# Performance work log

Hardware: AMD Instinct MI355X
Metric: run time of the kernel (lower is better)

## Reference

```python
import jax, jax.numpy as jnp
import numpy as np

N = 100_000      # nodes
E = 1_600_000    # edges (avg degree 16)
IN_DIM = 256
HID = 128
N_OUT = 2


def _linear_params(key, fan_in, fan_out):
    kw, kb = jax.random.split(key)
    bound = 1.0 / np.sqrt(fan_in)
    W = jax.random.uniform(kw, (fan_in, fan_out), jnp.float32, -bound, bound)
    b = jax.random.uniform(kb, (fan_out,), jnp.float32, -bound, bound)
    return W, b


def setup_inputs() -> dict:
    key = jax.random.key(0)
    ks = jax.random.split(key, 6)
    edge_index = jax.random.randint(ks[0], (2, E), 0, N, dtype=jnp.int64)
    x = jax.random.normal(ks[1], (N, IN_DIM), jnp.float32)
    Wi, bi = _linear_params(ks[2], IN_DIM, HID)   # NodeInitializer.lin
    W1, b1 = _linear_params(ks[3], HID, HID)      # GCNConv 1
    W2, b2 = _linear_params(ks[4], HID, HID)      # GCNConv 2
    Wh, bh = _linear_params(ks[5], HID, N_OUT)    # head
    return {"edge_index": edge_index, "x": x, "Wi": Wi, "bi": bi,
            "W1": W1, "b1": b1, "W2": W2, "b2": b2, "Wh": Wh, "bh": bh}


def reference(edge_index, x, Wi, bi, W1, b1, W2, b2, Wh, bh):
    n = x.shape[0]
    # GCNConv preprocessing: add self-loops, symmetric degree normalization.
    loops = jnp.arange(n, dtype=edge_index.dtype)
    src = jnp.concatenate([edge_index[0], loops])  # message source
    dst = jnp.concatenate([edge_index[1], loops])  # aggregation target
    deg = jax.ops.segment_sum(jnp.ones(src.shape[0], jnp.float32), dst, num_segments=n)
    dinv = jnp.where(deg > 0, deg ** -0.5, 0.0)
    norm = dinv[src] * dinv[dst]                   # [E+N]

    # NodeInitializer: relu(linear(x)); dropout = identity (eval mode)
    h = jax.nn.relu(x @ Wi + bi)

    # Two GCNConv layers (no relu between, matching SimpleGCN.forward)
    for W, b in ((W1, b1), (W2, b2)):
        msg = (h @ W)[src] * norm[:, None]         # gather + normalize, [E+N, HID]
        h = jax.ops.segment_sum(msg, dst, num_segments=n) + b  # scatter-add

    return h @ Wh + bh                             # [N, N_OUT]
```

## Files before the change

### kernel.cpp

```cpp
#include <hip/hip_runtime.h>
#include <hip/hip_bf16.h>

#define N_NODES 100000
#define N_EDGES 1600000
#define DIM_IN  256
#define DIM_H   128

#define NBKT 782
#define CPAD 16
#define EPB  8192
#define NBLK ((N_EDGES + EPB - 1) / EPB)

typedef __attribute__((ext_vector_type(8))) short short8;
typedef __attribute__((ext_vector_type(4))) float f32x4;

__device__ __forceinline__ int get_src(const int* e, int is64, int i) {
  return is64 ? e[2 * i] : e[i];
}
__device__ __forceinline__ int get_dst(const int* e, int is64, int i) {
  return is64 ? e[2 * (N_EDGES + i)] : e[N_EDGES + i];
}

__global__ __launch_bounds__(1024)
void k_init(const int* __restrict__ e, int* __restrict__ flag,
            int* __restrict__ bcnt) {
  if (blockIdx.x == 0) {
    __shared__ int s;
    if (threadIdx.x == 0) s = 0;
    __syncthreads();
    atomicOr(&s, e[2 * threadIdx.x + 1]);
    __syncthreads();
    if (threadIdx.x == 0) *flag = (s == 0) ? 1 : 0;
  } else {
    int i = (blockIdx.x - 1) * 1024 + threadIdx.x;
    if (i < NBKT * CPAD) bcnt[i] = 0;
  }
}

__global__ __launch_bounds__(256) void k_zero(int* __restrict__ p, int n) {
  int i = blockIdx.x * 256 + threadIdx.x;
  if (i < n) p[i] = 0;
}

__global__ __launch_bounds__(1024)
void k_binc(const int* __restrict__ eidx, const int* __restrict__ flag,
            int* __restrict__ bcnt) {
  __shared__ int hist[NBKT];
  const int t = threadIdx.x;
  const int is64 = *flag;
  for (int i = t; i < NBKT; i += 1024) hist[i] = 0;
  __syncthreads();
#pragma unroll
  for (int j = 0; j < EPB / 1024; ++j) {
    int e = blockIdx.x * EPB + j * 1024 + t;
    if (e < N_EDGES) {
      unsigned s = (unsigned)get_src(eidx, is64, e);
      unsigned d = (unsigned)get_dst(eidx, is64, e);
      if (s < N_NODES && d < N_NODES) atomicAdd(&hist[d >> 7], 1);
    }
  }
  __syncthreads();
  for (int i = t; i < NBKT; i += 1024) {
    int h = hist[i];
    if (h) atomicAdd(&bcnt[i * CPAD], h);
  }
}

__global__ __launch_bounds__(1024)
void k_bscan(int* __restrict__ bcnt, int* __restrict__ bbase) {
  __shared__ int sm[1024];
  int t = threadIdx.x;
  int v = (t < NBKT) ? bcnt[t * CPAD] : 0;
  sm[t] = v;
  __syncthreads();
  for (int d = 1; d < 1024; d <<= 1) {
    int u = (t >= d) ? sm[t - d] : 0;
    __syncthreads();
    sm[t] += u;
    __syncthreads();
  }
  if (t < NBKT) {
    int excl = sm[t] - v;
    bbase[t] = excl;
    bcnt[t * CPAD] = excl;
    if (t == NBKT - 1) bbase[NBKT] = sm[t];
  }
}

__global__ __launch_bounds__(1024)
void k_bin(const int* __restrict__ eidx, const int* __restrict__ flag,
           int* __restrict__ bcnt, unsigned* __restrict__ ebuf) {
  __shared__ int hist[NBKT];
  __shared__ int cur[NBKT];
  const int t = threadIdx.x;
  const int is64 = *flag;
  for (int i = t; i < NBKT; i += 1024) hist[i] = 0;
  unsigned rec[EPB / 1024];
  int bkt[EPB / 1024];
  __syncthreads();
#pragma unroll
  for (int j = 0; j < EPB / 1024; ++j) {
    int e = blockIdx.x * EPB + j * 1024 + t;
    bkt[j] = -1;
    rec[j] = 0;
    if (e < N_EDGES) {
      unsigned s = (unsigned)get_src(eidx, is64, e);
      unsigned d = (unsigned)get_dst(eidx, is64, e);
      if (s < N_NODES && d < N_NODES) {
        bkt[j] = (int)(d >> 7);
        rec[j] = s | ((d & 127u) << 17);
        atomicAdd(&hist[bkt[j]], 1);
      }
    }
  }
  __syncthreads();
  for (int i = t; i < NBKT; i += 1024) {
    int h = hist[i];
    cur[i] = h ? atomicAdd(&bcnt[i * CPAD], h) : 0;
  }
  __syncthreads();
#pragma unroll
  for (int j = 0; j < EPB / 1024; ++j) {
    if (bkt[j] >= 0) {
      int pos = atomicAdd(&cur[bkt[j]], 1);
      ebuf[pos] = rec[j];
    }
  }
}

__global__ __launch_bounds__(256)
void k_csr(const int* __restrict__ bbase, const unsigned* __restrict__ ebuf,
           int* __restrict__ off, float* __restrict__ dinv,
           int* __restrict__ csr) {
  __shared__ int hist[128];
  __shared__ int scn[128];
  __shared__ int cur[128];
  const int b = blockIdx.x, t = threadIdx.x;
  const int n0 = b << 7;
  const int start = bbase[b], end = bbase[b + 1];
  if (t < 128) hist[t] = 0;
  __syncthreads();
  for (int i = start + t; i < end; i += 256) {
    atomicAdd(&hist[ebuf[i] >> 17], 1);
  }
  __syncthreads();
  if (t < 128) scn[t] = hist[t];
  __syncthreads();
  for (int d = 1; d < 128; d <<= 1) {
    int u = (t < 128 && t >= d) ? scn[t - d] : 0;
    __syncthreads();
    if (t < 128) scn[t] += u;
    __syncthreads();
  }
  if (t < 128) {
    int node = n0 + t;
    if (node < N_NODES) {
      off[node] = start + scn[t];
      dinv[node] = rsqrtf(1.0f + (float)hist[t]);
      cur[t] = start + scn[t] - hist[t];
    }
  }
  __syncthreads();
  for (int i = start + t; i < end; i += 256) {
    unsigned r = ebuf[i];
    int pos = atomicAdd(&cur[r >> 17], 1);
    csr[pos] = (int)(r & 0x1FFFFu);
  }
}

__device__ __forceinline__ ushort f2bf(float f) {
  unsigned u = __float_as_uint(f);
  unsigned r = (u + 0x7fffu + ((u >> 16) & 1u)) >> 16;
  return (ushort)r;
}
__device__ __forceinline__ float bf2f(ushort h) {
  return __uint_as_float(((unsigned)h) << 16);
}

__device__ __forceinline__ void load8(const float* p, float* o) {
  float4 a = reinterpret_cast<const float4*>(p)[0];
  float4 b = reinterpret_cast<const float4*>(p)[1];
  o[0] = a.x; o[1] = a.y; o[2] = a.z; o[3] = a.w;
  o[4] = b.x; o[5] = b.y; o[6] = b.z; o[7] = b.w;
}

__device__ __forceinline__ void cvt_split(const float* v, short8& h, short8& l) {
#pragma unroll
  for (int j = 0; j < 8; ++j) {
    ushort hb = f2bf(v[j]);
    ushort lb = f2bf(v[j] - bf2f(hb));
    h[j] = (short)hb;
    l[j] = (short)lb;
  }
}

__global__ __launch_bounds__(256)
void k_prep(const float* __restrict__ Wi, const float* __restrict__ W1,
            const float* __restrict__ W2, const float* __restrict__ Wh,
            const float* __restrict__ b1, const float* __restrict__ b2,
            const float* __restrict__ bh, ushort* __restrict__ outHi,
            float* __restrict__ Wcc) {
  __shared__ float Wc2s[DIM_H][2];
  constexpr int CH = DIM_IN / 32;
  if (blockIdx.x == 16) {
    const int t = threadIdx.x;
    const int i = t >> 1, j = t & 1;
    float s = 0.f;
#pragma unroll 4
    for (int m = 0; m < DIM_H; ++m) s += W2[(size_t)i * DIM_H + m] * Wh[m * 2 + j];
    Wc2s[i][j] = s;
    __syncthreads();
    float c = 0.f;
#pragma unroll 4
    for (int k = 0; k < DIM_H; ++k) c += W1[(size_t)i * DIM_H + k] * Wc2s[k][j];
    Wcc[i * 2 + j] = c;
    if (t < 2) {
      float a = 0.f, b = 0.f;
      for (int k = 0; k < DIM_H; ++k) {
        a += b1[k] * Wc2s[k][t];
        b += b2[k] * Wh[k * 2 + t];
      }
      Wcc[256 + t] = a;
      Wcc[258 + t] = b + bh[t];
    }
    return;
  }
  int idx = blockIdx.x * 256 + threadIdx.x;
  int n  = idx & 15;
  int qq = (idx >> 4) & 3;
  int nt = (idx >> 6) & 7;
  int c  = idx >> 9;
  int col = nt * 16 + n;
  short8 h8, l8;
#pragma unroll
  for (int j = 0; j < 8; ++j) {
    float v = Wi[(size_t)(c * 32 + qq * 8 + j) * DIM_H + col];
    ushort hb = f2bf(v);
    ushort lb = f2bf(v - bf2f(hb));
    h8[j] = (short)hb;
    l8[j] = (short)lb;
  }
  ((short8*)outHi)[idx] = h8;
  ((short8*)outHi)[CH * 512 + idx] = l8;
}

template <int K>
__global__ __launch_bounds__(256, 3)
void k_gemm_xz(const float* __restrict__ A, const ushort* __restrict__ Bfrag,
               const float* __restrict__ bias, const float* __restrict__ Wcc,
               const float* __restrict__ dinv, float4* __restrict__ tbl) {
  constexpr int CH = K / 32;
  __shared__ __align__(16) ushort AhiS[2][512 * 8];
  __shared__ __align__(16) ushort AloS[2][512 * 8];
  const int tid = threadIdx.x;
  const int m0 = blockIdx.x * 128;
  const int wave = tid >> 6, lane = tid & 63;
  const int m_l = lane & 15, quad = lane >> 4;
  const int rs = tid >> 2, q = tid & 3;

  f32x4 acc[2][8];
#pragma unroll
  for (int i = 0; i < 2; ++i)
#pragma unroll
    for (int j = 0; j < 8; ++j) acc[i][j] = (f32x4){0.f, 0.f, 0.f, 0.f};

  const short8* Bhi8 = (const short8*)Bfrag;
  const short8* Blo8 = Bhi8 + CH * 512;
  short8* Ah = (short8*)AhiS;
  short8* Al = (short8*)AloS;

  const int gr0 = m0 + rs, gr1 = m0 + rs + 64;
  const float* Ap0 = &A[(size_t)((gr0 < N_NODES) ? gr0 : (N_NODES - 1)) * K + q * 8];
  const float* Ap1 = &A[(size_t)((gr1 < N_NODES) ? gr1 : (N_NODES - 1)) * K + q * 8];
  const int ent0 = (rs >> 4) * 64 + q * 16 + (rs & 15);
  const int ent1 = ent0 + 256;

  {
    float v0[8], v1[8];
    load8(Ap0, v0);
    load8(Ap1, v1);
    short8 h, l;
    cvt_split(v0, h, l);
    Ah[ent0] = h; Al[ent0] = l;
    cvt_split(v1, h, l);
    Ah[ent1] = h; Al[ent1] = l;
  }
  __syncthreads();

#pragma unroll
  for (int c = 0; c < CH; ++c) {
    const int cur = c & 1, nxt = cur ^ 1;
    float v0n[8], v1n[8];
    if (c + 1 < CH) {
      load8(Ap0 + (c + 1) * 32, v0n);
      load8(Ap1 + (c + 1) * 32, v1n);
    }
    const int bent0 = ((c * 8 + wave * 2 + 0) * 4 + quad) * 16 + m_l;
    const int bent1 = ((c * 8 + wave * 2 + 1) * 4 + quad) * 16 + m_l;
    short8 bhi0 = Bhi8[bent0], blo0 = Blo8[bent0];
    short8 bhi1 = Bhi8[bent1], blo1 = Blo8[bent1];
    const short8* AhC = Ah + cur * 512;
    const short8* AlC = Al + cur * 512;
#pragma unroll
    for (int mt = 0; mt < 8; ++mt) {
      short8 ahi = AhC[mt * 64 + quad * 16 + m_l];
      short8 alo = AlC[mt * 64 + quad * 16 + m_l];
      acc[0][mt] = __builtin_amdgcn_mfma_f32_16x16x32_bf16(ahi, bhi0, acc[0][mt], 0, 0, 0);
      acc[0][mt] = __builtin_amdgcn_mfma_f32_16x16x32_bf16(ahi, blo0, acc[0][mt], 0, 0, 0);
      acc[0][mt] = __builtin_amdgcn_mfma_f32_16x16x32_bf16(alo, bhi0, acc[0][mt], 0, 0, 0);
      acc[1][mt] = __builtin_amdgcn_mfma_f32_16x16x32_bf16(ahi, bhi1, acc[1][mt], 0, 0, 0);
      acc[1][mt] = __builtin_amdgcn_mfma_f32_16x16x32_bf16(ahi, blo1, acc[1][mt], 0, 0, 0);
      acc[1][mt] = __builtin_amdgcn_mfma_f32_16x16x32_bf16(alo, bhi1, acc[1][mt], 0, 0, 0);
    }
    if (c + 1 < CH) {
      short8 h, l;
      cvt_split(v0n, h, l);
      Ah[nxt * 512 + ent0] = h; Al[nxt * 512 + ent0] = l;
      cvt_split(v1n, h, l);
      Ah[nxt * 512 + ent1] = h; Al[nxt * 512 + ent1] = l;
    }
    __syncthreads();
  }

  float p0[8][4], p1[8][4];
#pragma unroll
  for (int mt = 0; mt < 8; ++mt)
#pragma unroll
    for (int r = 0; r < 4; ++r) { p0[mt][r] = 0.f; p1[mt][r] = 0.f; }
#pragma unroll
  for (int ntl = 0; ntl < 2; ++ntl) {
    const int colg = (wave * 2 + ntl) * 16 + m_l;
    const float bv = bias[colg];
    const float w0 = Wcc[colg * 2 + 0];
    const float w1 = Wcc[colg * 2 + 1];
#pragma unroll
    for (int mt = 0; mt < 8; ++mt)
#pragma unroll
      for (int r = 0; r < 4; ++r) {
        float hv = fmaxf(acc[ntl][mt][r] + bv, 0.f);
        p0[mt][r] += hv * w0;
        p1[mt][r] += hv * w1;
      }
  }
#pragma unroll
  for (int o = 1; o < 16; o <<= 1) {
#pragma unroll
    for (int mt = 0; mt < 8; ++mt)
#pragma unroll
      for (int r = 0; r < 4; ++r) {
        p0[mt][r] += __shfl_xor(p0[mt][r], o);
        p1[mt][r] += __shfl_xor(p1[mt][r], o);
      }
  }
  float* zred = (float*)AhiS;
  if (m_l == 0) {
#pragma unroll
    for (int mt = 0; mt < 8; ++mt)
#pragma unroll
      for (int r = 0; r < 4; ++r) {
        zred[(((0 * 4 + wave) * 4 + quad) * 8 + mt) * 4 + r] = p0[mt][r];
        zred[(((1 * 4 + wave) * 4 + quad) * 8 + mt) * 4 + r] = p1[mt][r];
      }
  }
  __syncthreads();
  if (tid < 128) {
    const int mt = tid >> 4, qd = (tid >> 2) & 3, r = tid & 3;
    const int rowg = m0 + tid;
    if (rowg < N_NODES) {
      float s0 = 0.f, s1 = 0.f;
#pragma unroll
      for (int w = 0; w < 4; ++w) {
        s0 += zred[(((0 * 4 + w) * 4 + qd) * 8 + mt) * 4 + r];
        s1 += zred[(((1 * 4 + w) * 4 + qd) * 8 + mt) * 4 + r];
      }
      float dn = dinv[rowg];
      tbl[rowg] = make_float4(dn * s0, dn * s1, dn, 0.f);
    }
  }
}

__global__ __launch_bounds__(256)
void k_aggr1(const int* __restrict__ off, const int* __restrict__ csr,
             const float4* __restrict__ tbl, float2* __restrict__ tb2,
             float* __restrict__ g) {
  int node = blockIdx.x * 256 + threadIdx.x;
  if (node >= N_NODES) return;
  int start = (node == 0) ? 0 : off[node - 1];
  int end = off[node];
  float4 self = tbl[node];
  float s0 = self.x, s1 = self.y, sd = self.z;
  int e = start;
  for (; e + 3 < end; e += 4) {
    int i0 = csr[e], i1 = csr[e + 1], i2 = csr[e + 2], i3 = csr[e + 3];
    float4 v0 = tbl[i0];
    float4 v1 = tbl[i1];
    float4 v2 = tbl[i2];
    float4 v3 = tbl[i3];
    s0 += (v0.x + v1.x) + (v2.x + v3.x);
    s1 += (v0.y + v1.y) + (v2.y + v3.y);
    sd += (v0.z + v1.z) + (v2.z + v3.z);
  }
  for (; e < end; ++e) {
    float4 v = tbl[csr[e]];
    s0 += v.x; s1 += v.y; sd += v.z;
  }
  float dn = self.z;
  tb2[node] = make_float2(dn * dn * s0, dn * dn * s1);
  g[node] = dn * sd;
}

__global__ __launch_bounds__(256)
void k_aggr2(const int* __restrict__ off, const int* __restrict__ csr,
             const float2* __restrict__ tb2, const float* __restrict__ dinv,
             const float* __restrict__ g, const float* __restrict__ tail,
             float* __restrict__ out) {
  int node = blockIdx.x * 256 + threadIdx.x;
  if (node >= N_NODES) return;
  int start = (node == 0) ? 0 : off[node - 1];
  int end = off[node];
  float2 self = tb2[node];
  float s0 = self.x, s1 = self.y;
  int e = start;
  for (; e + 3 < end; e += 4) {
    int i0 = csr[e], i1 = csr[e + 1], i2 = csr[e + 2], i3 = csr[e + 3];
    float2 v0 = tb2[i0];
    float2 v1 = tb2[i1];
    float2 v2 = tb2[i2];
    float2 v3 = tb2[i3];
    s0 += (v0.x + v1.x) + (v2.x + v3.x);
    s1 += (v0.y + v1.y) + (v2.y + v3.y);
  }
  for (; e < end; ++e) {
    float2 v = tb2[csr[e]];
    s0 += v.x; s1 += v.y;
  }
  float dn = dinv[node], gv = g[node];
  float o0 = dn * s0 + gv * tail[0] + tail[2];
  float o1 = dn * s1 + gv * tail[1] + tail[3];
  reinterpret_cast<float2*>(out)[node] = make_float2(o0, o1);
}

__global__ __launch_bounds__(256) void k_count(const int* __restrict__ eidx,
                                               const int* __restrict__ flag,
                                               int* __restrict__ off) {
  int e = blockIdx.x * 256 + threadIdx.x;
  int is64 = *flag;
  if (e < N_EDGES) {
    unsigned d = (unsigned)get_dst(eidx, is64, e);
    if (d < N_NODES) atomicAdd(&off[d], 1);
  }
}

__global__ __launch_bounds__(256) void k_dinv_old(const int* __restrict__ off,
                                                  float* __restrict__ dinv) {
  int i = blockIdx.x * 256 + threadIdx.x;
  if (i < N_NODES) dinv[i] = rsqrtf(1.0f + (float)off[i]);
}

template <int K>
__global__ __launch_bounds__(256)
void k_gemm(const float* __restrict__ A, const float* __restrict__ B,
            const float* __restrict__ bias, const float* __restrict__ scale,
            float* __restrict__ C, const int do_relu) {
  __shared__ float As[64][33];
  const int tid = threadIdx.x;
  const int tx = tid & 15;
  const int ty = tid >> 4;
  const int m0 = blockIdx.x * 64;

  float acc[4][8];
#pragma unroll
  for (int i = 0; i < 4; ++i)
#pragma unroll
    for (int j = 0; j < 8; ++j) acc[i][j] = 0.f;

  const int rs = tid >> 2;
  const int ks = (tid & 3) * 8;

  for (int k0 = 0; k0 < K; k0 += 32) {
    float av8[8];
    const int gm = m0 + rs;
    if (gm < N_NODES) {
      load8(&A[(size_t)gm * K + k0 + ks], av8);
    } else {
#pragma unroll
      for (int j = 0; j < 8; ++j) av8[j] = 0.f;
    }
    __syncthreads();
#pragma unroll
    for (int j = 0; j < 8; ++j) As[rs][ks + j] = av8[j];
    __syncthreads();

    const float* Bp = B + (size_t)k0 * DIM_H + tx * 8;
#pragma unroll 4
    for (int k = 0; k < 32; ++k) {
      float bv[8];
      load8(Bp + (size_t)k * DIM_H, bv);
      float av[4];
#pragma unroll
      for (int rr = 0; rr < 4; ++rr) av[rr] = As[ty * 4 + rr][k];
#pragma unroll
      for (int rr = 0; rr < 4; ++rr)
#pragma unroll
        for (int cc = 0; cc < 8; ++cc)
          acc[rr][cc] = fmaf(av[rr], bv[cc], acc[rr][cc]);
    }
  }

  float bs[8];
  if (bias) {
    load8(bias + tx * 8, bs);
  } else {
#pragma unroll
    for (int j = 0; j < 8; ++j) bs[j] = 0.f;
  }
#pragma unroll
  for (int rr = 0; rr < 4; ++rr) {
    const int gm = m0 + ty * 4 + rr;
    if (gm < N_NODES) {
      float sc = scale ? scale[gm] : 1.0f;
      float v[8];
#pragma unroll
      for (int cc = 0; cc < 8; ++cc) {
        float t = acc[rr][cc] + bs[cc];
        if (do_relu) t = fmaxf(t, 0.f);
        v[cc] = t * sc;
      }
      float* Cp = &C[(size_t)gm * DIM_H + tx * 8];
      reinterpret_cast<float4*>(Cp)[0] = make_float4(v[0], v[1], v[2], v[3]);
      reinterpret_cast<float4*>(Cp)[1] = make_float4(v[4], v[5], v[6], v[7]);
    }
  }
}

__global__ __launch_bounds__(256)
void k_aggr_init(const float* __restrict__ t, const float* __restrict__ dinv,
                 const float* __restrict__ bias, float* __restrict__ h) {
  int idx = blockIdx.x * 256 + threadIdx.x;
  if (idx < N_NODES * DIM_H) {
    int i = idx >> 7;
    int c = idx & 127;
    float d = dinv[i];
    h[idx] = bias[c] + t[idx] * d * d;
  }
}

__global__ __launch_bounds__(256)
void k_aggr_edges(const int* __restrict__ eidx, const int* __restrict__ flag,
                  const float* __restrict__ t, const float* __restrict__ dinv,
                  float* __restrict__ h) {
  int e = blockIdx.x * 2 + (threadIdx.x >> 7);
  int c = threadIdx.x & 127;
  int is64 = *flag;
  if (e < N_EDGES) {
    unsigned s = (unsigned)get_src(eidx, is64, e);
    unsigned d = (unsigned)get_dst(eidx, is64, e);
    if (s < N_NODES && d < N_NODES) {
      float nrm = dinv[s] * dinv[d];
      unsafeAtomicAdd(&h[(size_t)d * DIM_H + c], t[(size_t)s * DIM_H + c] * nrm);
    }
  }
}

__global__ __launch_bounds__(256)
void k_head_f32(const float* __restrict__ h, const float* __restrict__ Wh,
                const float* __restrict__ bh, float* __restrict__ out) {
  int node = blockIdx.x * 4 + (threadIdx.x >> 6);
  int lane = threadIdx.x & 63;
  if (node >= N_NODES) return;
  float h0 = h[(size_t)node * DIM_H + lane];
  float h1 = h[(size_t)node * DIM_H + 64 + lane];
  float s0 = h0 * Wh[lane * 2 + 0] + h1 * Wh[(lane + 64) * 2 + 0];
  float s1 = h0 * Wh[lane * 2 + 1] + h1 * Wh[(lane + 64) * 2 + 1];
#pragma unroll
  for (int off = 32; off > 0; off >>= 1) {
    s0 += __shfl_down(s0, off);
    s1 += __shfl_down(s1, off);
  }
  if (lane == 0) {
    reinterpret_cast<float2*>(out)[node] = make_float2(s0 + bh[0], s1 + bh[1]);
  }
}

extern "C" void kernel_launch(void* const* d_in, const int* in_sizes, int n_in,
                              void* d_out, int out_size, void* d_ws, size_t ws_size,
                              hipStream_t stream) {
  (void)in_sizes; (void)n_in; (void)out_size;
  const int* eidx = (const int*)d_in[0];
  const float* x  = (const float*)d_in[1];
  const float* Wi = (const float*)d_in[2];
  const float* bi = (const float*)d_in[3];
  const float* W1 = (const float*)d_in[4];
  const float* b1 = (const float*)d_in[5];
  const float* W2 = (const float*)d_in[6];
  const float* b2 = (const float*)d_in[7];
  const float* Wh = (const float*)d_in[8];
  const float* bh = (const float*)d_in[9];
  float* out = (float*)d_out;

  const int gE  = (N_EDGES + 255) / 256;
  const int gM  = (N_NODES + 63) / 64;
  const int gM2 = (N_NODES + 127) / 128;
  const int gW  = (N_NODES + 3) / 4;
  const int gN256 = (N_NODES + 255) / 256;

  char* ws = (char*)d_ws;
  int* flag = (int*)ws;

  const size_t need1 = 17410048;

  if (ws_size >= need1) {
    int*      bcnt  = (int*)(ws + 4096);
    int*      bbase = (int*)(ws + 57344);
    float*    Wcc   = (float*)(ws + 61440);
    ushort*   bfWi  = (ushort*)(ws + 65536);
    int*      off   = (int*)(ws + 262144);
    float*    dinv  = (float*)(ws + 720896);
    float*    g     = (float*)(ws + 1179648);
    float4*   tbl   = (float4*)(ws + 1638400);
    float2*   tb2   = (float2*)(ws + 3407872);
    int*      csr   = (int*)(ws + 4456448);
    unsigned* ebuf  = (unsigned*)(ws + 11010048);

    k_init<<<1 + (NBKT * CPAD + 1023) / 1024, 1024, 0, stream>>>(eidx, flag, bcnt);
    k_binc<<<NBLK, 1024, 0, stream>>>(eidx, flag, bcnt);
    k_bscan<<<1, 1024, 0, stream>>>(bcnt, bbase);
    k_bin<<<NBLK, 1024, 0, stream>>>(eidx, flag, bcnt, ebuf);
    k_csr<<<NBKT, 256, 0, stream>>>(bbase, ebuf, off, dinv, csr);

    k_prep<<<17, 256, 0, stream>>>(Wi, W1, W2, Wh, b1, b2, bh, bfWi, Wcc);

    k_gemm_xz<DIM_IN><<<gM2, 256, 0, stream>>>(x, bfWi, bi, Wcc, dinv, tbl);
    k_aggr1<<<gN256, 256, 0, stream>>>(off, csr, tbl, tb2, g);
    k_aggr2<<<gN256, 256, 0, stream>>>(off, csr, tb2, dinv, g, Wcc + 256, out);
  } else {
    const int gN  = (N_NODES + 255) / 256;
    int*   off  = (int*)(ws + 4096);
    float* dinv = (float*)(ws + 404480);
    float* fbA  = (float*)(ws + 804864);
    float* fbB  = (float*)(ws + 804864 + (size_t)N_NODES * DIM_H * 4);
    const int gNH = (N_NODES * DIM_H + 255) / 256;
    const int gE2 = (N_EDGES + 1) / 2;
    k_init<<<1, 1024, 0, stream>>>(eidx, flag, (int*)(ws + 4096));
    k_zero<<<gN, 256, 0, stream>>>(off, N_NODES);
    k_count<<<gE, 256, 0, stream>>>(eidx, flag, off);
    k_dinv_old<<<gN, 256, 0, stream>>>(off, dinv);

    k_gemm<DIM_IN><<<gM, 256, 0, stream>>>(x, Wi, bi, nullptr, fbA, 1);
    k_gemm<DIM_H><<<gM, 256, 0, stream>>>(fbA, W1, nullptr, nullptr, fbB, 0);
    k_aggr_init<<<gNH, 256, 0, stream>>>(fbB, dinv, b1, fbA);
    k_aggr_edges<<<gE2, 256, 0, stream>>>(eidx, flag, fbB, dinv, fbA);
    k_gemm<DIM_H><<<gM, 256, 0, stream>>>(fbA, W2, nullptr, nullptr, fbB, 0);
    k_aggr_init<<<gNH, 256, 0, stream>>>(fbB, dinv, b2, fbA);
    k_aggr_edges<<<gE2, 256, 0, stream>>>(eidx, flag, fbB, dinv, fbA);
    k_head_f32<<<gW, 256, 0, stream>>>(fbA, Wh, bh, out);
  }
}
```

Baseline: 294.5 us.

## Halve GEMM row tile, swizzle LDS A layout, prefetch B fragments

Shrinks the x@Wi GEMM tile from 128 to 64 rows per block, doubling the grid and raising the occupancy hint to 4 blocks per CU. It XOR-swizzles the LDS write and read indices to reduce bank conflicts. It also register-prefetches the next chunk's B fragments alongside the next A chunk so they overlap with the MFMA work. The trade-off is less reuse of B per loaded fragment and more blocks re-reading the weights.

```diff
diff --git a/kernel.cpp b/kernel.cpp
--- a/kernel.cpp
+++ b/kernel.cpp
@@ -245,86 +245,88 @@
 }
 
 template <int K>
-__global__ __launch_bounds__(256, 3)
+__global__ __launch_bounds__(256, 4)
 void k_gemm_xz(const float* __restrict__ A, const ushort* __restrict__ Bfrag,
                const float* __restrict__ bias, const float* __restrict__ Wcc,
                const float* __restrict__ dinv, float4* __restrict__ tbl) {
   constexpr int CH = K / 32;
-  __shared__ __align__(16) ushort AhiS[2][512 * 8];
-  __shared__ __align__(16) ushort AloS[2][512 * 8];
+  __shared__ __align__(16) ushort AhiS[2][256 * 8];
+  __shared__ __align__(16) ushort AloS[2][256 * 8];
   const int tid = threadIdx.x;
-  const int m0 = blockIdx.x * 128;
+  const int m0 = blockIdx.x * 64;
   const int wave = tid >> 6, lane = tid & 63;
   const int m_l = lane & 15, quad = lane >> 4;
   const int rs = tid >> 2, q = tid & 3;
 
-  f32x4 acc[2][8];
+  f32x4 acc[2][4];
 #pragma unroll
   for (int i = 0; i < 2; ++i)
 #pragma unroll
-    for (int j = 0; j < 8; ++j) acc[i][j] = (f32x4){0.f, 0.f, 0.f, 0.f};
+    for (int j = 0; j < 4; ++j) acc[i][j] = (f32x4){0.f, 0.f, 0.f, 0.f};
 
   const short8* Bhi8 = (const short8*)Bfrag;
   const short8* Blo8 = Bhi8 + CH * 512;
   short8* Ah = (short8*)AhiS;
   short8* Al = (short8*)AloS;
 
-  const int gr0 = m0 + rs, gr1 = m0 + rs + 64;
-  const float* Ap0 = &A[(size_t)((gr0 < N_NODES) ? gr0 : (N_NODES - 1)) * K + q * 8];
-  const float* Ap1 = &A[(size_t)((gr1 < N_NODES) ? gr1 : (N_NODES - 1)) * K + q * 8];
-  const int ent0 = (rs >> 4) * 64 + q * 16 + (rs & 15);
-  const int ent1 = ent0 + 256;
+  const int gr = m0 + rs;
+  const float* Ap = &A[(size_t)((gr < N_NODES) ? gr : (N_NODES - 1)) * K + q * 8];
+  const int went = (rs >> 4) * 64 + q * 16 + ((rs & 15) ^ (q << 2));
+  const int rent = quad * 16 + (m_l ^ (quad << 2));
 
   {
-    float v0[8], v1[8];
-    load8(Ap0, v0);
-    load8(Ap1, v1);
+    float v[8];
+    load8(Ap, v);
     short8 h, l;
-    cvt_split(v0, h, l);
-    Ah[ent0] = h; Al[ent0] = l;
-    cvt_split(v1, h, l);
-    Ah[ent1] = h; Al[ent1] = l;
-  }
+    cvt_split(v, h, l);
+    Ah[went] = h;
+    Al[went] = l;
+  }
+  const int bq = quad * 16 + m_l;
+  short8 bh0 = Bhi8[(wave * 2 + 0) * 64 + bq];
+  short8 bl0 = Blo8[(wave * 2 + 0) * 64 + bq];
+  short8 bh1 = Bhi8[(wave * 2 + 1) * 64 + bq];
+  short8 bl1 = Blo8[(wave * 2 + 1) * 64 + bq];
   __syncthreads();
 
 #pragma unroll
   for (int c = 0; c < CH; ++c) {
     const int cur = c & 1, nxt = cur ^ 1;
-    float v0n[8], v1n[8];
+    float vn[8];
+    short8 nbh0, nbl0, nbh1, nbl1;
     if (c + 1 < CH) {
-      load8(Ap0 + (c + 1) * 32, v0n);
-      load8(Ap1 + (c + 1) * 32, v1n);
-    }
-    const int bent0 = ((c * 8 + wave * 2 + 0) * 4 + quad) * 16 + m_l;
-    const int bent1 = ((c * 8 + wave * 2 + 1) * 4 + quad) * 16 + m_l;
-    short8 bhi0 = Bhi8[bent0], blo0 = Blo8[bent0];
-    short8 bhi1 = Bhi8[bent1], blo1 = Blo8[bent1];
-    const short8* AhC = Ah + cur * 512;
-    const short8* AlC = Al + cur * 512;
-#pragma unroll
-    for (int mt = 0; mt < 8; ++mt) {
-      short8 ahi = AhC[mt * 64 + quad * 16 + m_l];
-      short8 alo = AlC[mt * 64 + quad * 16 + m_l];
-      acc[0][mt] = __builtin_amdgcn_mfma_f32_16x16x32_bf16(ahi, bhi0, acc[0][mt], 0, 0, 0);
-      acc[0][mt] = __builtin_amdgcn_mfma_f32_16x16x32_bf16(ahi, blo0, acc[0][mt], 0, 0, 0);
-      acc[0][mt] = __builtin_amdgcn_mfma_f32_16x16x32_bf16(alo, bhi0, acc[0][mt], 0, 0, 0);
-      acc[1][mt] = __builtin_amdgcn_mfma_f32_16x16x32_bf16(ahi, bhi1, acc[1][mt], 0, 0, 0);
-      acc[1][mt] = __builtin_amdgcn_mfma_f32_16x16x32_bf16(ahi, blo1, acc[1][mt], 0, 0, 0);
-      acc[1][mt] = __builtin_amdgcn_mfma_f32_16x16x32_bf16(alo, bhi1, acc[1][mt], 0, 0, 0);
+      load8(Ap + (c + 1) * 32, vn);
+      const int b0 = ((c + 1) * 8 + wave * 2 + 0) * 64 + bq;
+      const int b1 = ((c + 1) * 8 + wave * 2 + 1) * 64 + bq;
+      nbh0 = Bhi8[b0]; nbl0 = Blo8[b0];
+      nbh1 = Bhi8[b1]; nbl1 = Blo8[b1];
+    }
+    const short8* AhC = Ah + cur * 256;
+    const short8* AlC = Al + cur * 256;
+#pragma unroll
+    for (int mt = 0; mt < 4; ++mt) {
+      short8 ahi = AhC[mt * 64 + rent];
+      short8 alo = AlC[mt * 64 + rent];
+      acc[0][mt] = __builtin_amdgcn_mfma_f32_16x16x32_bf16(ahi, bh0, acc[0][mt], 0, 0, 0);
+      acc[0][mt] = __builtin_amdgcn_mfma_f32_16x16x32_bf16(ahi, bl0, acc[0][mt], 0, 0, 0);
+      acc[0][mt] = __builtin_amdgcn_mfma_f32_16x16x32_bf16(alo, bh0, acc[0][mt], 0, 0, 0);
+      acc[1][mt] = __builtin_amdgcn_mfma_f32_16x16x32_bf16(ahi, bh1, acc[1][mt], 0, 0, 0);
+      acc[1][mt] = __builtin_amdgcn_mfma_f32_16x16x32_bf16(ahi, bl1, acc[1][mt], 0, 0, 0);
+      acc[1][mt] = __builtin_amdgcn_mfma_f32_16x16x32_bf16(alo, bh1, acc[1][mt], 0, 0, 0);
     }
     if (c + 1 < CH) {
       short8 h, l;
-      cvt_split(v0n, h, l);
-      Ah[nxt * 512 + ent0] = h; Al[nxt * 512 + ent0] = l;
-      cvt_split(v1n, h, l);
-      Ah[nxt * 512 + ent1] = h; Al[nxt * 512 + ent1] = l;
-    }
-    __syncthreads();
-  }
-
-  float p0[8][4], p1[8][4];
-#pragma unroll
-  for (int mt = 0; mt < 8; ++mt)
+      cvt_split(vn, h, l);
+      Ah[nxt * 256 + went] = h;
+      Al[nxt * 256 + went] = l;
+      bh0 = nbh0; bl0 = nbl0; bh1 = nbh1; bl1 = nbl1;
+    }
+    __syncthreads();
+  }
+
+  float p0[4][4], p1[4][4];
+#pragma unroll
+  for (int mt = 0; mt < 4; ++mt)
 #pragma unroll
     for (int r = 0; r < 4; ++r) { p0[mt][r] = 0.f; p1[mt][r] = 0.f; }
 #pragma unroll
@@ -334,7 +336,7 @@
     const float w0 = Wcc[colg * 2 + 0];
     const float w1 = Wcc[colg * 2 + 1];
 #pragma unroll
-    for (int mt = 0; mt < 8; ++mt)
+    for (int mt = 0; mt < 4; ++mt)
 #pragma unroll
       for (int r = 0; r < 4; ++r) {
         float hv = fmaxf(acc[ntl][mt][r] + bv, 0.f);
@@ -345,7 +347,7 @@
 #pragma unroll
   for (int o = 1; o < 16; o <<= 1) {
 #pragma unroll
-    for (int mt = 0; mt < 8; ++mt)
+    for (int mt = 0; mt < 4; ++mt)
 #pragma unroll
       for (int r = 0; r < 4; ++r) {
         p0[mt][r] += __shfl_xor(p0[mt][r], o);
@@ -355,23 +357,23 @@
   float* zred = (float*)AhiS;
   if (m_l == 0) {
 #pragma unroll
-    for (int mt = 0; mt < 8; ++mt)
+    for (int mt = 0; mt < 4; ++mt)
 #pragma unroll
       for (int r = 0; r < 4; ++r) {
-        zred[(((0 * 4 + wave) * 4 + quad) * 8 + mt) * 4 + r] = p0[mt][r];
-        zred[(((1 * 4 + wave) * 4 + quad) * 8 + mt) * 4 + r] = p1[mt][r];
+        zred[(((0 * 4 + wave) * 4 + quad) * 4 + mt) * 4 + r] = p0[mt][r];
+        zred[(((1 * 4 + wave) * 4 + quad) * 4 + mt) * 4 + r] = p1[mt][r];
       }
   }
   __syncthreads();
-  if (tid < 128) {
+  if (tid < 64) {
     const int mt = tid >> 4, qd = (tid >> 2) & 3, r = tid & 3;
     const int rowg = m0 + tid;
     if (rowg < N_NODES) {
       float s0 = 0.f, s1 = 0.f;
 #pragma unroll
       for (int w = 0; w < 4; ++w) {
-        s0 += zred[(((0 * 4 + w) * 4 + qd) * 8 + mt) * 4 + r];
-        s1 += zred[(((1 * 4 + w) * 4 + qd) * 8 + mt) * 4 + r];
+        s0 += zred[(((0 * 4 + w) * 4 + qd) * 4 + mt) * 4 + r];
+        s1 += zred[(((1 * 4 + w) * 4 + qd) * 4 + mt) * 4 + r];
       }
       float dn = dinv[rowg];
       tbl[rowg] = make_float4(dn * s0, dn * s1, dn, 0.f);
@@ -600,7 +602,6 @@
 
   const int gE  = (N_EDGES + 255) / 256;
   const int gM  = (N_NODES + 63) / 64;
-  const int gM2 = (N_NODES + 127) / 128;
   const int gW  = (N_NODES + 3) / 4;
   const int gN256 = (N_NODES + 255) / 256;
 
@@ -630,7 +631,7 @@
 
     k_prep<<<17, 256, 0, stream>>>(Wi, W1, W2, Wh, b1, b2, bh, bfWi, Wcc);
 
-    k_gemm_xz<DIM_IN><<<gM2, 256, 0, stream>>>(x, bfWi, bi, Wcc, dinv, tbl);
+    k_gemm_xz<DIM_IN><<<gM, 256, 0, stream>>>(x, bfWi, bi, Wcc, dinv, tbl);
     k_aggr1<<<gN256, 256, 0, stream>>>(off, csr, tbl, tb2, g);
     k_aggr2<<<gN256, 256, 0, stream>>>(off, csr, tb2, dinv, g, Wcc + 256, out);
   } else {
```

Measured after the change: 285.3 us. -3.1%, faster.
